# Performance work log

Measured on AMD Instinct MI355X. Metric: run time of the kernel, lower is better.

Reference implementation:

```python
import jax, jax.numpy as jnp
import numpy as np

C, H, W, NC, LC = 512, 160, 160, 1203, 64


def setup_inputs() -> dict:
    key = jax.random.key(0)
    ks = jax.random.split(key, 8)
    return {
        "cls_feat": jax.random.normal(ks[0], (1, C, H, W), jnp.float32),
        "loc_feat": jax.random.normal(ks[1], (1, LC, H, W), jnp.float32),
        "conf": jax.random.uniform(ks[2], (1,), jnp.float32, 0.2, 0.8),
        "pf_w": jax.random.normal(ks[3], (C,), jnp.float32) * 0.02,   # pf 1x1 conv, C->1
        "pf_b": jnp.zeros((1,), jnp.float32),
        "vocab_w": jax.random.normal(ks[4], (NC, C), jnp.float32) * 0.02,  # conv2linear weight
        "vocab_b": jnp.zeros((NC,), jnp.float32),
        "loc_w": jax.random.normal(ks[5], (LC, LC), jnp.float32) * 0.02,   # loc 1x1 conv
        "loc_b": jnp.zeros((LC,), jnp.float32),
    }


def reference(cls_feat, loc_feat, conf, pf_w, pf_b, vocab_w, vocab_b, loc_w, loc_b):
    B, Cc, Hh, Ww = cls_feat.shape
    # proposal-filter score: 1x1 conv C->1 on batch 0, flattened to [HW]
    pf_score = jnp.einsum('c,chw->hw', pf_w, cls_feat[0]).reshape(-1) + pf_b  # [HW]
    mask = jax.nn.sigmoid(pf_score) > conf[0]  # [HW] bool
    # tokens: [1, HW, C]
    tok = cls_feat.reshape(B, Cc, Hh * Ww).transpose(0, 2, 1)
    # static-shape equivalent of the proposal filter: zero masked-out tokens
    tok = tok * mask[None, :, None].astype(tok.dtype)
    # vocab linear (converted 1x1 conv): [1, HW, NC] -> [1, NC, HW]
    cls_out = (jnp.einsum('bnc,vc->bnv', tok, vocab_w) + vocab_b).transpose(0, 2, 1)
    # localization 1x1 conv
    loc_out = jnp.einsum('oi,bihw->bohw', loc_w, loc_feat) + loc_b[None, :, None, None]
    return loc_out, cls_out, mask
```

## Files before the change

kernel.cpp:

```cpp
#include <hip/hip_runtime.h>
#include <math.h>


constexpr int C_    = 512;
constexpr int HW_   = 25600;
constexpr int NC_   = 1203;
constexpr int VPAD_ = 1216;

constexpr int LOC_OFF_  = 0;
constexpr int CLS_OFF_  = 64 * HW_;
constexpr int MASK_OFF_ = CLS_OFF_ + NC_ * HW_;

constexpr int PF_BLOCKS_    = HW_ / 64;
constexpr int LOC_BLOCKS_   = 400;
constexpr int FILL_BLOCKS_  = 2048;
constexpr int TRANS_BLOCKS_ = 19 * 8;

typedef float vfloat4 __attribute__((ext_vector_type(4)));

__global__ void k_init(int* cnt) { *cnt = 0; }

__global__ __launch_bounds__(256) void k_main(
    const float* __restrict__ cls_feat, const float* __restrict__ loc_feat,
    const float* __restrict__ conf, const float* __restrict__ pf_w,
    const float* __restrict__ pf_b, const float* __restrict__ vocab_w,
    const float* __restrict__ vocab_b, const float* __restrict__ loc_w,
    const float* __restrict__ loc_b, float* __restrict__ out,
    int* __restrict__ cnt, int* __restrict__ idxList,
    float* __restrict__ AT4, int jcap)
{
    const int bid = blockIdx.x;
    const int tid = threadIdx.x;

    if (bid < PF_BLOCKS_) {
        __shared__ double sPart[256];
        const int hwi   = tid & 63;
        const int slice = tid >> 6;
        const int hw    = bid * 64 + hwi;
        const float* p  = cls_feat + (size_t)slice * 128 * HW_ + hw;
        const float* w  = pf_w + slice * 128;
        double acc = 0.0;
        #pragma unroll 4
        for (int k = 0; k < 128; ++k)
            acc += (double)w[k] * (double)p[(size_t)k * HW_];
        sPart[tid] = acc;
        __syncthreads();
        if (slice == 0) {
            double s = sPart[hwi] + sPart[64 + hwi] + sPart[128 + hwi] +
                       sPart[192 + hwi] + (double)pf_b[0];
            double sig = 1.0 / (1.0 + exp(-s));
            bool m = sig > (double)conf[0];
            out[MASK_OFF_ + hw] = m ? 1.0f : 0.0f;
            if (m) {
                int pos = atomicAdd(cnt, 1);
                if (pos < HW_) idxList[pos] = hw;
            }
        }
    } else if (bid < PF_BLOCKS_ + LOC_BLOCKS_) {
        const int j   = bid - PF_BLOCKS_;
        const int hwb = j % 100;
        const int o0  = (j / 100) * 16;
        __shared__ float sw[16][64];
        for (int i = tid; i < 16 * 64; i += 256)
            sw[i >> 6][i & 63] = loc_w[(o0 + (i >> 6)) * 64 + (i & 63)];
        __syncthreads();
        const int hw = hwb * 256 + tid;
        float acc[16];
        #pragma unroll
        for (int r = 0; r < 16; ++r) acc[r] = loc_b[o0 + r];
        for (int i = 0; i < 64; ++i) {
            float f = loc_feat[(size_t)i * HW_ + hw];
            #pragma unroll
            for (int r = 0; r < 16; ++r) acc[r] += sw[r][i] * f;
        }
        #pragma unroll
        for (int r = 0; r < 16; ++r)
            out[LOC_OFF_ + (size_t)(o0 + r) * HW_ + hw] = acc[r];
    } else if (bid < PF_BLOCKS_ + LOC_BLOCKS_ + FILL_BLOCKS_) {
        const int fb = bid - PF_BLOCKS_ - LOC_BLOCKS_;
        const int total4 = NC_ * HW_ / 4;
        vfloat4* o = (vfloat4*)(out + CLS_OFF_);
        for (int i = fb * 256 + tid; i < total4; i += FILL_BLOCKS_ * 256) {
            int v = i / (HW_ / 4);
            float b = vocab_b[v];
            vfloat4 val = {b, b, b, b};
            __builtin_nontemporal_store(val, &o[i]);
        }
    } else {
        if (jcap <= 0) return;
        const int tb = bid - PF_BLOCKS_ - LOC_BLOCKS_ - FILL_BLOCKS_;
        const int v0 = (tb % 19) * 64;
        const int k0 = (tb / 19) * 64;
        __shared__ float t[64][65];
        const int c  = tid & 63;
        const int r4 = tid >> 6;
        #pragma unroll
        for (int i = 0; i < 16; ++i) {
            const int r = r4 * 16 + i;
            const int v = v0 + r;
            t[r][c] = (v < NC_) ? vocab_w[(size_t)v * C_ + k0 + c] : 0.f;
        }
        __syncthreads();
        #pragma unroll
        for (int i = 0; i < 16; ++i) {
            const int k  = r4 * 16 + i;
            const int kg = k0 + k;
            AT4[((size_t)(kg >> 2) * VPAD_ + v0 + c) * 4 + (kg & 3)] = t[c][k];
        }
    }
}

__global__ __launch_bounds__(256) void k_gatherJ(
    const float* __restrict__ cls_feat, const int* __restrict__ cnt,
    const int* __restrict__ idxList, float* __restrict__ BdT, int jcap)
{
    const int count = min(*cnt, HW_);
    if (count > jcap) return;
    const int t = threadIdx.x;
    for (int j = blockIdx.x; j < count; j += gridDim.x) {
        const int hw = idxList[j];
        BdT[(size_t)j * C_ + t]       = cls_feat[(size_t)t * HW_ + hw];
        BdT[(size_t)j * C_ + 256 + t] = cls_feat[(size_t)(256 + t) * HW_ + hw];
    }
}

__global__ __launch_bounds__(256) void k_gemm6x(
    const float* __restrict__ AT4, const float* __restrict__ vocab_b,
    const int* __restrict__ cnt, const int* __restrict__ idxList,
    const float* __restrict__ BdT, float* __restrict__ out, int jcap)
{
    const int count = min(*cnt, HW_);
    if (count == 0 || count > jcap) return;

    const int slot = blockIdx.y;
    const int vt   = blockIdx.x + 8 * (slot % 3);
    if (vt >= 19) return;
    const int jBase = (slot / 3) * 4;
    if (jBase >= count) return;

    const int tid  = threadIdx.x;
    const int lane = tid & 63;
    const int w    = __builtin_amdgcn_readfirstlane(tid >> 6);
    const int v0   = vt * 64;
    const int v    = v0 + lane;
    const float* __restrict__ Acol = AT4 + (size_t)v * 4;

    const int j0 = jBase + 0, j1 = jBase + 1, j2 = jBase + 2, j3 = jBase + 3;
    const float* __restrict__ B0 = BdT + (size_t)(j0 < count ? j0 : 0) * C_;
    const float* __restrict__ B1 = BdT + (size_t)(j1 < count ? j1 : 0) * C_;
    const float* __restrict__ B2 = BdT + (size_t)(j2 < count ? j2 : 0) * C_;
    const float* __restrict__ B3 = BdT + (size_t)(j3 < count ? j3 : 0) * C_;

    vfloat4 ac0 = {0,0,0,0}, ac1 = {0,0,0,0}, ac2 = {0,0,0,0}, ac3 = {0,0,0,0};
    const int kqBeg = w * 32;
    #pragma unroll 8
    for (int q = 0; q < 32; ++q) {
        const int kq = kqBeg + q;
        const vfloat4 a  = *(const vfloat4*)(Acol + (size_t)kq * VPAD_ * 4);
        const vfloat4 b0 = *(const vfloat4*)(B0 + kq * 4);
        const vfloat4 b1 = *(const vfloat4*)(B1 + kq * 4);
        const vfloat4 b2 = *(const vfloat4*)(B2 + kq * 4);
        const vfloat4 b3 = *(const vfloat4*)(B3 + kq * 4);
        ac0 += a * b0; ac1 += a * b1; ac2 += a * b2; ac3 += a * b3;
    }

    __shared__ float sRed[4][4][64];
    sRed[w][0][lane] = (ac0.x + ac0.y) + (ac0.z + ac0.w);
    sRed[w][1][lane] = (ac1.x + ac1.y) + (ac1.z + ac1.w);
    sRed[w][2][lane] = (ac2.x + ac2.y) + (ac2.z + ac2.w);
    sRed[w][3][lane] = (ac3.x + ac3.y) + (ac3.z + ac3.w);
    __syncthreads();

    if (tid < 64 && v < NC_) {
        const float bias = vocab_b[v];
        #pragma unroll
        for (int jj = 0; jj < 4; ++jj) {
            const int j = jBase + jj;
            if (j < count) {
                const float s =
                    (sRed[0][jj][lane] + sRed[1][jj][lane]) +
                    (sRed[2][jj][lane] + sRed[3][jj][lane]);
                const int hw = idxList[j];
                out[CLS_OFF_ + (size_t)v * HW_ + hw] = s + bias;
            }
        }
    }
}

__global__ __launch_bounds__(256) void k_gemm_fallback(
    const float* __restrict__ cls_feat, const float* __restrict__ vocab_w,
    const float* __restrict__ vocab_b, const int* __restrict__ cnt,
    const int* __restrict__ idxList, float* __restrict__ out, int capB)
{
    const int count = min(*cnt, HW_);
    if (count <= capB) return;
    const int v0 = blockIdx.x * 64;

    __shared__ float sAT[16][64];
    __shared__ float sBT[16][64];
    __shared__ int   sIdx[64];

    const int tid = threadIdx.x;
    const int tx = tid & 15;
    const int ty = tid >> 4;
    const int r  = tid >> 2;
    const int kq = tid & 3;

    for (int jb = blockIdx.y; (jb << 6) < count; jb += gridDim.y) {
        const int j0 = jb << 6;
        __syncthreads();
        if (tid < 64) {
            int j = j0 + tid;
            sIdx[tid] = (j < count) ? idxList[j] : -1;
        }
        __syncthreads();
        const int hwj = sIdx[r];

        float acc[4][4] = {};
        for (int k0 = 0; k0 < C_; k0 += 16) {
            float4 a4 = make_float4(0.f, 0.f, 0.f, 0.f);
            if (v0 + r < NC_)
                a4 = *(const float4*)(vocab_w + (size_t)(v0 + r) * C_ + k0 + kq * 4);
            float b0 = 0.f, b1 = 0.f, b2 = 0.f, b3 = 0.f;
            if (hwj >= 0) {
                const float* bp = cls_feat + (size_t)(k0 + kq * 4) * HW_ + hwj;
                b0 = bp[0]; b1 = bp[HW_]; b2 = bp[2 * HW_]; b3 = bp[3 * HW_];
            }
            __syncthreads();
            sAT[kq * 4 + 0][r] = a4.x; sAT[kq * 4 + 1][r] = a4.y;
            sAT[kq * 4 + 2][r] = a4.z; sAT[kq * 4 + 3][r] = a4.w;
            sBT[kq * 4 + 0][r] = b0;   sBT[kq * 4 + 1][r] = b1;
            sBT[kq * 4 + 2][r] = b2;   sBT[kq * 4 + 3][r] = b3;
            __syncthreads();
            #pragma unroll
            for (int kk = 0; kk < 16; ++kk) {
                const float4 av = *(const float4*)&sAT[kk][ty * 4];
                const float4 bv = *(const float4*)&sBT[kk][tx * 4];
                acc[0][0] += av.x * bv.x; acc[0][1] += av.x * bv.y;
                acc[0][2] += av.x * bv.z; acc[0][3] += av.x * bv.w;
                acc[1][0] += av.y * bv.x; acc[1][1] += av.y * bv.y;
                acc[1][2] += av.y * bv.z; acc[1][3] += av.y * bv.w;
                acc[2][0] += av.z * bv.x; acc[2][1] += av.z * bv.y;
                acc[2][2] += av.z * bv.z; acc[2][3] += av.z * bv.w;
                acc[3][0] += av.w * bv.x; acc[3][1] += av.w * bv.y;
                acc[3][2] += av.w * bv.z; acc[3][3] += av.w * bv.w;
            }
        }
        #pragma unroll
        for (int a = 0; a < 4; ++a) {
            int v = v0 + ty * 4 + a;
            if (v >= NC_) continue;
            float bias = vocab_b[v];
            #pragma unroll
            for (int b = 0; b < 4; ++b) {
                int j = j0 + tx * 4 + b;
                if (j < count) {
                    int hw = sIdx[tx * 4 + b];
                    out[CLS_OFF_ + (size_t)v * HW_ + hw] = acc[a][b] + bias;
                }
            }
        }
    }
}

extern "C" void kernel_launch(void* const* d_in, const int* in_sizes, int n_in,
                              void* d_out, int out_size, void* d_ws,
                              size_t ws_size, hipStream_t stream) {
    const float* cls_feat = (const float*)d_in[0];
    const float* loc_feat = (const float*)d_in[1];
    const float* conf     = (const float*)d_in[2];
    const float* pf_w     = (const float*)d_in[3];
    const float* pf_b     = (const float*)d_in[4];
    const float* vocab_w  = (const float*)d_in[5];
    const float* vocab_b  = (const float*)d_in[6];
    const float* loc_w    = (const float*)d_in[7];
    const float* loc_b    = (const float*)d_in[8];
    float* out = (float*)d_out;

    int*   cnt     = (int*)d_ws;
    int*   idxList = (int*)((char*)d_ws + 4096);
    size_t fixed   = 4096 + (size_t)HW_ * sizeof(int);
    size_t atBytes = (size_t)(C_ / 4) * VPAD_ * 4 * sizeof(float);
    float* AT4     = (float*)((char*)d_ws + fixed);
    float* BdT     = (float*)((char*)d_ws + fixed + atBytes);

    int jcap = 0;
    if (ws_size > fixed + atBytes) {
        size_t cols = (ws_size - fixed - atBytes) / ((size_t)C_ * sizeof(float));
        jcap = (int)(cols > 1024 ? 1024 : cols);
        jcap &= ~63;
    }

    hipLaunchKernelGGL(k_init, dim3(1), dim3(1), 0, stream, cnt);
    hipLaunchKernelGGL(k_main,
                       dim3(PF_BLOCKS_ + LOC_BLOCKS_ + FILL_BLOCKS_ +
                            TRANS_BLOCKS_),
                       dim3(256), 0, stream,
                       cls_feat, loc_feat, conf, pf_w, pf_b, vocab_w, vocab_b,
                       loc_w, loc_b, out, cnt, idxList, AT4, jcap);
    if (jcap > 0) {
        hipLaunchKernelGGL(k_gatherJ, dim3(512), dim3(256), 0, stream,
                           cls_feat, cnt, idxList, BdT, jcap);
        hipLaunchKernelGGL(k_gemm6x, dim3(8, 768), dim3(256), 0, stream,
                           AT4, vocab_b, cnt, idxList, BdT, out, jcap);
    }
    hipLaunchKernelGGL(k_gemm_fallback, dim3((NC_ + 63) / 64, 8), dim3(256),
                       0, stream, cls_feat, vocab_w, vocab_b, cnt, idxList,
                       out, jcap);
}
```

Measured before the change: 62.07 us.

## Merge main, gather and dense GEMM into one cooperative persistent kernel

Combines the proposal-filter, transpose, loc conv, bias fill, gather and small dense GEMM into a single cooperative kernel of 512 persistent blocks, using grid-wide syncs in place of separate launches. The counter init becomes a memset. The aim is to cut launch overhead and inter-kernel gaps. The cost is that each phase now runs on a fixed grid of 512 blocks, so the fill and PF phases lose parallelism, and grid.sync adds barrier latency.

```diff
diff --git a/kernel.cpp b/kernel.cpp
--- a/kernel.cpp
+++ b/kernel.cpp
@@ -1,5 +1,8 @@
 #include <hip/hip_runtime.h>
+#include <hip/hip_cooperative_groups.h>
 #include <math.h>
+
+namespace cg = cooperative_groups;
 
 
 constexpr int C_    = 512;
@@ -11,43 +14,50 @@
 constexpr int CLS_OFF_  = 64 * HW_;
 constexpr int MASK_OFF_ = CLS_OFF_ + NC_ * HW_;
 
-constexpr int PF_BLOCKS_    = HW_ / 64;
-constexpr int LOC_BLOCKS_   = 400;
-constexpr int FILL_BLOCKS_  = 2048;
-constexpr int TRANS_BLOCKS_ = 19 * 8;
+constexpr int PF_N_    = 400;
+constexpr int TRANS_N_ = 152;
+constexpr int LOC_N_   = 400;
+constexpr int GRID_    = 512;
 
 typedef float vfloat4 __attribute__((ext_vector_type(4)));
 
-__global__ void k_init(int* cnt) { *cnt = 0; }
-
-__global__ __launch_bounds__(256) void k_main(
+__global__ __launch_bounds__(256, 2) void k_coop(
     const float* __restrict__ cls_feat, const float* __restrict__ loc_feat,
     const float* __restrict__ conf, const float* __restrict__ pf_w,
     const float* __restrict__ pf_b, const float* __restrict__ vocab_w,
     const float* __restrict__ vocab_b, const float* __restrict__ loc_w,
     const float* __restrict__ loc_b, float* __restrict__ out,
     int* __restrict__ cnt, int* __restrict__ idxList,
-    float* __restrict__ AT4, int jcap)
+    float* __restrict__ AT4, float* __restrict__ BdT, int jcap)
 {
+    cg::grid_group grid = cg::this_grid();
     const int bid = blockIdx.x;
     const int tid = threadIdx.x;
 
-    if (bid < PF_BLOCKS_) {
-        __shared__ double sPart[256];
+    __shared__ union {
+        double sPart[256];
+        float  sw[16][64];
+        float  tt[64][65];
+        float  red[4][4][64];
+    } sh;
+
+    if (bid < PF_N_) {
+        const int t     = bid;
         const int hwi   = tid & 63;
         const int slice = tid >> 6;
-        const int hw    = bid * 64 + hwi;
+        const int hw    = t * 64 + hwi;
         const float* p  = cls_feat + (size_t)slice * 128 * HW_ + hw;
         const float* w  = pf_w + slice * 128;
         double acc = 0.0;
         #pragma unroll 4
         for (int k = 0; k < 128; ++k)
             acc += (double)w[k] * (double)p[(size_t)k * HW_];
-        sPart[tid] = acc;
+        sh.sPart[tid] = acc;
         __syncthreads();
         if (slice == 0) {
-            double s = sPart[hwi] + sPart[64 + hwi] + sPart[128 + hwi] +
-                       sPart[192 + hwi] + (double)pf_b[0];
+            double s = sh.sPart[hwi] + sh.sPart[64 + hwi] +
+                       sh.sPart[128 + hwi] + sh.sPart[192 + hwi] +
+                       (double)pf_b[0];
             double sig = 1.0 / (1.0 + exp(-s));
             bool m = sig > (double)conf[0];
             out[MASK_OFF_ + hw] = m ? 1.0f : 0.0f;
@@ -56,13 +66,58 @@
                 if (pos < HW_) idxList[pos] = hw;
             }
         }
-    } else if (bid < PF_BLOCKS_ + LOC_BLOCKS_) {
-        const int j   = bid - PF_BLOCKS_;
+    } else if (bid < PF_N_ + 112 && jcap > 0) {
+        const int tb = bid - PF_N_;
+        const int v0 = (tb % 19) * 64;
+        const int k0 = (tb / 19) * 64;
+        const int c  = tid & 63;
+        const int r4 = tid >> 6;
+        #pragma unroll
+        for (int i = 0; i < 16; ++i) {
+            const int r = r4 * 16 + i;
+            const int v = v0 + r;
+            sh.tt[r][c] = (v < NC_) ? vocab_w[(size_t)v * C_ + k0 + c] : 0.f;
+        }
+        __syncthreads();
+        #pragma unroll
+        for (int i = 0; i < 16; ++i) {
+            const int k  = r4 * 16 + i;
+            const int kg = k0 + k;
+            AT4[((size_t)(kg >> 2) * VPAD_ + v0 + c) * 4 + (kg & 3)] =
+                sh.tt[c][k];
+        }
+    }
+    __syncthreads();
+
+    const int idx2 = bid + GRID_;
+    if (idx2 < PF_N_ + TRANS_N_) {
+        if (jcap > 0) {
+            const int tb = idx2 - PF_N_;
+            const int v0 = (tb % 19) * 64;
+            const int k0 = (tb / 19) * 64;
+            const int c  = tid & 63;
+            const int r4 = tid >> 6;
+            #pragma unroll
+            for (int i = 0; i < 16; ++i) {
+                const int r = r4 * 16 + i;
+                const int v = v0 + r;
+                sh.tt[r][c] = (v < NC_) ? vocab_w[(size_t)v * C_ + k0 + c] : 0.f;
+            }
+            __syncthreads();
+            #pragma unroll
+            for (int i = 0; i < 16; ++i) {
+                const int k  = r4 * 16 + i;
+                const int kg = k0 + k;
+                AT4[((size_t)(kg >> 2) * VPAD_ + v0 + c) * 4 + (kg & 3)] =
+                    sh.tt[c][k];
+            }
+        }
+    } else if (idx2 < PF_N_ + TRANS_N_ + LOC_N_) {
+        const int j   = idx2 - PF_N_ - TRANS_N_;
         const int hwb = j % 100;
         const int o0  = (j / 100) * 16;
-        __shared__ float sw[16][64];
         for (int i = tid; i < 16 * 64; i += 256)
-            sw[i >> 6][i & 63] = loc_w[(o0 + (i >> 6)) * 64 + (i & 63)];
+            sh.sw[i >> 6][i & 63] = loc_w[(o0 + (i >> 6)) * 64 + (i & 63)];
         __syncthreads();
         const int hw = hwb * 256 + tid;
         float acc[16];
@@ -71,117 +126,91 @@
         for (int i = 0; i < 64; ++i) {
             float f = loc_feat[(size_t)i * HW_ + hw];
             #pragma unroll
-            for (int r = 0; r < 16; ++r) acc[r] += sw[r][i] * f;
+            for (int r = 0; r < 16; ++r) acc[r] += sh.sw[r][i] * f;
         }
         #pragma unroll
         for (int r = 0; r < 16; ++r)
             out[LOC_OFF_ + (size_t)(o0 + r) * HW_ + hw] = acc[r];
-    } else if (bid < PF_BLOCKS_ + LOC_BLOCKS_ + FILL_BLOCKS_) {
-        const int fb = bid - PF_BLOCKS_ - LOC_BLOCKS_;
+    }
+    __syncthreads();
+
+    {
         const int total4 = NC_ * HW_ / 4;
         vfloat4* o = (vfloat4*)(out + CLS_OFF_);
-        for (int i = fb * 256 + tid; i < total4; i += FILL_BLOCKS_ * 256) {
+        for (int i = bid * 256 + tid; i < total4; i += GRID_ * 256) {
             int v = i / (HW_ / 4);
             float b = vocab_b[v];
             vfloat4 val = {b, b, b, b};
             __builtin_nontemporal_store(val, &o[i]);
         }
-    } else {
-        if (jcap <= 0) return;
-        const int tb = bid - PF_BLOCKS_ - LOC_BLOCKS_ - FILL_BLOCKS_;
-        const int v0 = (tb % 19) * 64;
-        const int k0 = (tb / 19) * 64;
-        __shared__ float t[64][65];
-        const int c  = tid & 63;
-        const int r4 = tid >> 6;
-        #pragma unroll
-        for (int i = 0; i < 16; ++i) {
-            const int r = r4 * 16 + i;
-            const int v = v0 + r;
-            t[r][c] = (v < NC_) ? vocab_w[(size_t)v * C_ + k0 + c] : 0.f;
-        }
-        __syncthreads();
-        #pragma unroll
-        for (int i = 0; i < 16; ++i) {
-            const int k  = r4 * 16 + i;
-            const int kg = k0 + k;
-            AT4[((size_t)(kg >> 2) * VPAD_ + v0 + c) * 4 + (kg & 3)] = t[c][k];
-        }
-    }
-}
-
-__global__ __launch_bounds__(256) void k_gatherJ(
-    const float* __restrict__ cls_feat, const int* __restrict__ cnt,
-    const int* __restrict__ idxList, float* __restrict__ BdT, int jcap)
-{
+    }
+
+    grid.sync();
+
     const int count = min(*cnt, HW_);
-    if (count > jcap) return;
-    const int t = threadIdx.x;
-    for (int j = blockIdx.x; j < count; j += gridDim.x) {
-        const int hw = idxList[j];
-        BdT[(size_t)j * C_ + t]       = cls_feat[(size_t)t * HW_ + hw];
-        BdT[(size_t)j * C_ + 256 + t] = cls_feat[(size_t)(256 + t) * HW_ + hw];
-    }
-}
-
-__global__ __launch_bounds__(256) void k_gemm6x(
-    const float* __restrict__ AT4, const float* __restrict__ vocab_b,
-    const int* __restrict__ cnt, const int* __restrict__ idxList,
-    const float* __restrict__ BdT, float* __restrict__ out, int jcap)
-{
-    const int count = min(*cnt, HW_);
-    if (count == 0 || count > jcap) return;
-
-    const int slot = blockIdx.y;
-    const int vt   = blockIdx.x + 8 * (slot % 3);
-    if (vt >= 19) return;
-    const int jBase = (slot / 3) * 4;
-    if (jBase >= count) return;
-
-    const int tid  = threadIdx.x;
-    const int lane = tid & 63;
-    const int w    = __builtin_amdgcn_readfirstlane(tid >> 6);
-    const int v0   = vt * 64;
-    const int v    = v0 + lane;
-    const float* __restrict__ Acol = AT4 + (size_t)v * 4;
-
-    const int j0 = jBase + 0, j1 = jBase + 1, j2 = jBase + 2, j3 = jBase + 3;
-    const float* __restrict__ B0 = BdT + (size_t)(j0 < count ? j0 : 0) * C_;
-    const float* __restrict__ B1 = BdT + (size_t)(j1 < count ? j1 : 0) * C_;
-    const float* __restrict__ B2 = BdT + (size_t)(j2 < count ? j2 : 0) * C_;
-    const float* __restrict__ B3 = BdT + (size_t)(j3 < count ? j3 : 0) * C_;
-
-    vfloat4 ac0 = {0,0,0,0}, ac1 = {0,0,0,0}, ac2 = {0,0,0,0}, ac3 = {0,0,0,0};
-    const int kqBeg = w * 32;
-    #pragma unroll 8
-    for (int q = 0; q < 32; ++q) {
-        const int kq = kqBeg + q;
-        const vfloat4 a  = *(const vfloat4*)(Acol + (size_t)kq * VPAD_ * 4);
-        const vfloat4 b0 = *(const vfloat4*)(B0 + kq * 4);
-        const vfloat4 b1 = *(const vfloat4*)(B1 + kq * 4);
-        const vfloat4 b2 = *(const vfloat4*)(B2 + kq * 4);
-        const vfloat4 b3 = *(const vfloat4*)(B3 + kq * 4);
-        ac0 += a * b0; ac1 += a * b1; ac2 += a * b2; ac3 += a * b3;
-    }
-
-    __shared__ float sRed[4][4][64];
-    sRed[w][0][lane] = (ac0.x + ac0.y) + (ac0.z + ac0.w);
-    sRed[w][1][lane] = (ac1.x + ac1.y) + (ac1.z + ac1.w);
-    sRed[w][2][lane] = (ac2.x + ac2.y) + (ac2.z + ac2.w);
-    sRed[w][3][lane] = (ac3.x + ac3.y) + (ac3.z + ac3.w);
-    __syncthreads();
-
-    if (tid < 64 && v < NC_) {
-        const float bias = vocab_b[v];
-        #pragma unroll
-        for (int jj = 0; jj < 4; ++jj) {
-            const int j = jBase + jj;
-            if (j < count) {
-                const float s =
-                    (sRed[0][jj][lane] + sRed[1][jj][lane]) +
-                    (sRed[2][jj][lane] + sRed[3][jj][lane]);
-                const int hw = idxList[j];
-                out[CLS_OFF_ + (size_t)v * HW_ + hw] = s + bias;
+    const bool dense = (jcap > 0) && (count > 0) && (count <= jcap);
+    if (dense) {
+        for (int j = bid; j < count; j += GRID_) {
+            const int hw = idxList[j];
+            BdT[(size_t)j * C_ + tid] = cls_feat[(size_t)tid * HW_ + hw];
+            BdT[(size_t)j * C_ + 256 + tid] =
+                cls_feat[(size_t)(256 + tid) * HW_ + hw];
+        }
+    }
+
+    grid.sync();
+
+    if (dense) {
+        const int lane = tid & 63;
+        const int w    = __builtin_amdgcn_readfirstlane(tid >> 6);
+        const int ngt  = 19 * ((count + 3) >> 2);
+        for (int t = bid; t < ngt; t += GRID_) {
+            const int vt    = t % 19;
+            const int jBase = (t / 19) * 4;
+            const int v0    = vt * 64;
+            const int v     = v0 + lane;
+            const float* __restrict__ Acol = AT4 + (size_t)v * 4;
+
+            const int j0 = jBase, j1 = jBase + 1, j2 = jBase + 2, j3 = jBase + 3;
+            const float* __restrict__ B0 = BdT + (size_t)(j0 < count ? j0 : 0) * C_;
+            const float* __restrict__ B1 = BdT + (size_t)(j1 < count ? j1 : 0) * C_;
+            const float* __restrict__ B2 = BdT + (size_t)(j2 < count ? j2 : 0) * C_;
+            const float* __restrict__ B3 = BdT + (size_t)(j3 < count ? j3 : 0) * C_;
+
+            vfloat4 ac0 = {0,0,0,0}, ac1 = {0,0,0,0};
+            vfloat4 ac2 = {0,0,0,0}, ac3 = {0,0,0,0};
+            const int kqBeg = w * 32;
+            #pragma unroll 8
+            for (int q = 0; q < 32; ++q) {
+                const int kq = kqBeg + q;
+                const vfloat4 a  = *(const vfloat4*)(Acol + (size_t)kq * VPAD_ * 4);
+                const vfloat4 b0 = *(const vfloat4*)(B0 + kq * 4);
+                const vfloat4 b1 = *(const vfloat4*)(B1 + kq * 4);
+                const vfloat4 b2 = *(const vfloat4*)(B2 + kq * 4);
+                const vfloat4 b3 = *(const vfloat4*)(B3 + kq * 4);
+                ac0 += a * b0; ac1 += a * b1; ac2 += a * b2; ac3 += a * b3;
+            }
+
+            __syncthreads();
+            sh.red[w][0][lane] = (ac0.x + ac0.y) + (ac0.z + ac0.w);
+            sh.red[w][1][lane] = (ac1.x + ac1.y) + (ac1.z + ac1.w);
+            sh.red[w][2][lane] = (ac2.x + ac2.y) + (ac2.z + ac2.w);
+            sh.red[w][3][lane] = (ac3.x + ac3.y) + (ac3.z + ac3.w);
+            __syncthreads();
+
+            if (tid < 64 && v < NC_) {
+                const float bias = vocab_b[v];
+                #pragma unroll
+                for (int jj = 0; jj < 4; ++jj) {
+                    const int j = jBase + jj;
+                    if (j < count) {
+                        const float s =
+                            (sh.red[0][jj][lane] + sh.red[1][jj][lane]) +
+                            (sh.red[2][jj][lane] + sh.red[3][jj][lane]);
+                        const int hw = idxList[j];
+                        out[CLS_OFF_ + (size_t)v * HW_ + hw] = s + bias;
+                    }
+                }
             }
         }
     }
@@ -291,19 +320,16 @@
         jcap &= ~63;
     }
 
-    hipLaunchKernelGGL(k_init, dim3(1), dim3(1), 0, stream, cnt);
-    hipLaunchKernelGGL(k_main,
-                       dim3(PF_BLOCKS_ + LOC_BLOCKS_ + FILL_BLOCKS_ +
-                            TRANS_BLOCKS_),
-                       dim3(256), 0, stream,
-                       cls_feat, loc_feat, conf, pf_w, pf_b, vocab_w, vocab_b,
-                       loc_w, loc_b, out, cnt, idxList, AT4, jcap);
-    if (jcap > 0) {
-        hipLaunchKernelGGL(k_gatherJ, dim3(512), dim3(256), 0, stream,
-                           cls_feat, cnt, idxList, BdT, jcap);
-        hipLaunchKernelGGL(k_gemm6x, dim3(8, 768), dim3(256), 0, stream,
-                           AT4, vocab_b, cnt, idxList, BdT, out, jcap);
-    }
+    hipMemsetAsync(cnt, 0, sizeof(int), stream);
+
+    void* args[] = {
+        (void*)&cls_feat, (void*)&loc_feat, (void*)&conf, (void*)&pf_w,
+        (void*)&pf_b, (void*)&vocab_w, (void*)&vocab_b, (void*)&loc_w,
+        (void*)&loc_b, (void*)&out, (void*)&cnt, (void*)&idxList,
+        (void*)&AT4, (void*)&BdT, (void*)&jcap };
+    hipLaunchCooperativeKernel((const void*)k_coop, dim3(GRID_), dim3(256),
+                               args, 0, stream);
+
     hipLaunchKernelGGL(k_gemm_fallback, dim3((NC_ + 63) / 64, 8), dim3(256),
                        0, stream, cls_feat, vocab_w, vocab_b, cnt, idxList,
                        out, jcap);
```

After: 230.3 us. 271% more time.
